# Kernel optimization log

Hardware: AMD Instinct MI355X
Metric: run time of the kernel (lower is better)

The kernel has to match this reference:

```python
import jax, jax.numpy as jnp
from jax import lax
import numpy as np


def _conv(x, w, b, stride=1, pad=1):
    # x: [B,C,H,W], w: [O,I,kh,kw]
    y = lax.conv_general_dilated(x, w, (stride, stride), [(pad, pad), (pad, pad)],
                                 dimension_numbers=('NCHW', 'OIHW', 'NCHW'))
    return y + b[None, :, None, None]


def _bn(x, g, b, eps=1e-5):
    # torch BatchNorm2d in training mode: per-channel batch stats, biased variance
    m = jnp.mean(x, axis=(0, 2, 3), keepdims=True)
    v = jnp.var(x, axis=(0, 2, 3), keepdims=True)
    return (x - m) * lax.rsqrt(v + eps) * g[None, :, None, None] + b[None, :, None, None]


def _res_stack(h, w1, b1, w2, b2):
    # one ResidualStack: layers of ReLU->conv3x3->ReLU->conv1x1 with skip, final ReLU
    for i in range(w1.shape[0]):
        t = jnp.maximum(_conv(jnp.maximum(h, 0.0), w1[i], b1[i], 1, 1), 0.0)
        h = h + _conv(t, w2[i], b2[i], 1, 0)
    return jnp.maximum(h, 0.0)


def reference(x, enc_conv0_w, enc_conv0_b, enc_bn0_g, enc_bn0_b, enc_conv1_w, enc_conv1_b,
              enc_bn1_g, enc_bn1_b, enc_conv2_w, enc_conv2_b, enc_res_w1, enc_res_b1,
              enc_res_w2, enc_res_b2, enc_conv3_w, enc_conv3_b, codebook,
              dec_conv0_w, dec_conv0_b, dec_res_w1, dec_res_b1, dec_res_w2, dec_res_b2,
              dec_conv1_w, dec_conv1_b, dec_deconv_w, dec_deconv_b):
    # ---- encoder ----
    h = jnp.maximum(_bn(_conv(x, enc_conv0_w, enc_conv0_b, 2, 1), enc_bn0_g, enc_bn0_b), 0.0)
    h = jnp.maximum(_bn(_conv(h, enc_conv1_w, enc_conv1_b, 1, 1), enc_bn1_g, enc_bn1_b), 0.0)
    h = _conv(h, enc_conv2_w, enc_conv2_b, 1, 1)
    for s in range(enc_res_w1.shape[0]):
        h = _res_stack(h, enc_res_w1[s], enc_res_b1[s], enc_res_w2[s], enc_res_b2[s])
    z = _conv(h, enc_conv3_w, enc_conv3_b, 1, 1)  # [B,D,H,W]
    # ---- vector quantizer ----
    Bz, D, H, W = z.shape
    zf = z.transpose(0, 2, 3, 1).reshape(-1, D)  # [N,D]
    d = (jnp.sum(zf * zf, axis=1, keepdims=True)
         - 2.0 * (zf @ codebook.T)
         + jnp.sum(codebook * codebook, axis=1))  # [N,K]
    idx = jnp.argmin(d, axis=1)
    q = codebook[idx]  # direct gather == one-hot @ codebook
    e_loss = jnp.mean((lax.stop_gradient(q) - zf) ** 2)
    q_loss = jnp.mean((q - lax.stop_gradient(zf)) ** 2)
    vq_loss = q_loss + 0.25 * e_loss
    qst = zf + lax.stop_gradient(q - zf)  # straight-through
    zq = qst.reshape(Bz, H, W, D).transpose(0, 3, 1, 2)
    # ---- decoder ----
    h = _conv(zq, dec_conv0_w, dec_conv0_b, 1, 1)
    for s in range(dec_res_w1.shape[0]):
        h = _res_stack(h, dec_res_w1[s], dec_res_b1[s], dec_res_w2[s], dec_res_b2[s])
    h = jnp.maximum(_conv(h, dec_conv1_w, dec_conv1_b, 1, 1), 0.0)
    # ConvTranspose2d(k=4,s=2,p=1): flip kernel, swap I/O, lhs_dilation=2, pad=k-1-p=2
    wt = jnp.transpose(jnp.flip(dec_deconv_w, (2, 3)), (1, 0, 2, 3))
    xr = lax.conv_general_dilated(h, wt, (1, 1), [(2, 2), (2, 2)], lhs_dilation=(2, 2),
                                  dimension_numbers=('NCHW', 'OIHW', 'NCHW'))
    xr = xr + dec_deconv_b[None, :, None, None]
    recon = jnp.mean((xr - x) ** 2)
    total = recon + vq_loss
    return xr, total, recon


def setup_inputs() -> dict:
    key = jax.random.key(0)
    ks = iter(jax.random.split(key, 64))

    def W(shape):
        fan_in = float(np.prod(shape[-3:]))
        return jax.random.normal(next(ks), shape, jnp.float32) / float(np.sqrt(fan_in))

    def Bv(shape):
        return 0.01 * jax.random.normal(next(ks), shape, jnp.float32)

    inp = {}
    inp['x'] = jax.random.normal(next(ks), (8, 3, 128, 128), jnp.float32)
    inp['enc_conv0_w'] = W((256, 3, 4, 4)); inp['enc_conv0_b'] = Bv((256,))
    inp['enc_bn0_g'] = 1.0 + 0.1 * jax.random.normal(next(ks), (256,), jnp.float32)
    inp['enc_bn0_b'] = Bv((256,))
    inp['enc_conv1_w'] = W((512, 256, 3, 3)); inp['enc_conv1_b'] = Bv((512,))
    inp['enc_bn1_g'] = 1.0 + 0.1 * jax.random.normal(next(ks), (512,), jnp.float32)
    inp['enc_bn1_b'] = Bv((512,))
    inp['enc_conv2_w'] = W((512, 512, 3, 3)); inp['enc_conv2_b'] = Bv((512,))
    inp['enc_res_w1'] = W((4, 4, 128, 512, 3, 3)); inp['enc_res_b1'] = Bv((4, 4, 128))
    inp['enc_res_w2'] = W((4, 4, 512, 128, 1, 1)); inp['enc_res_b2'] = Bv((4, 4, 512))
    inp['enc_conv3_w'] = W((256, 512, 3, 3)); inp['enc_conv3_b'] = Bv((256,))
    inp['codebook'] = jax.random.uniform(next(ks), (1024, 256), jnp.float32, -1.0 / 1024, 1.0 / 1024)
    inp['dec_conv0_w'] = W((512, 256, 3, 3)); inp['dec_conv0_b'] = Bv((512,))
    inp['dec_res_w1'] = W((4, 4, 128, 512, 3, 3)); inp['dec_res_b1'] = Bv((4, 4, 128))
    inp['dec_res_w2'] = W((4, 4, 512, 128, 1, 1)); inp['dec_res_b2'] = Bv((4, 4, 512))
    inp['dec_conv1_w'] = W((256, 512, 3, 3)); inp['dec_conv1_b'] = Bv((256,))
    inp['dec_deconv_w'] = W((256, 3, 4, 4)); inp['dec_deconv_b'] = Bv((3,))
    return inp
```

## Files before the change

kernel.cpp:

```cpp
#include <hip/hip_runtime.h>
#include <cstddef>

#define F_OUT_RELU   2
#define F_IN_BNORM   32
#define F_STATS      64

typedef __attribute__((ext_vector_type(8))) short short8;
typedef __attribute__((ext_vector_type(4))) short short4v;
typedef __attribute__((ext_vector_type(4))) float floatx4;

__device__ inline float bf2f(short h) {
  union { unsigned int u; float f; } v;
  v.u = ((unsigned int)(unsigned short)h) << 16;
  return v.f;
}
__device__ inline short f2bf(float f) {
  union { float f; unsigned int u; } v; v.f = f;
  unsigned int r = v.u + 0x7fffu + ((v.u >> 16) & 1u);
  return (short)(r >> 16);
}

__global__ void k_init(float* p) {
  for (int i = threadIdx.x; i < 1664; i += 256) p[i] = 0.f;
}

__global__ __launch_bounds__(256) void k_wswz(
    const float* __restrict__ w, short* __restrict__ wq,
    int Cin, int K2, int per_layer)
{
  int idx = blockIdx.x * 256 + threadIdx.x;
  if (idx >= per_layer) return;
  int layer = blockIdx.y;
  w  += (size_t)layer * per_layer;
  wq += (size_t)layer * per_layer;
  int nch = Cin >> 5;
  int j = idx & 7;
  int lane = (idx >> 3) & 63;
  int r = idx >> 9;
  int cich = r % nch; int r2 = r / nch;
  int kk = r2 % K2;   int co_grp = r2 / K2;
  int co = co_grp * 16 + (lane & 15);
  int ci = (cich << 5) + ((lane >> 4) << 3) + j;
  wq[idx] = f2bf(w[((size_t)co * Cin + ci) * K2 + kk]);
}

__global__ __launch_bounds__(256) void k_wswz0m(
    const float* __restrict__ w, short* __restrict__ wq)
{
  int idx = blockIdx.x * 256 + threadIdx.x;
  if (idx >= 16384) return;
  int co = idx >> 6, k = idx & 63;
  float val = (k < 48) ? w[co * 48 + k] : 0.f;
  int cich = k >> 5;
  int lane = (((k >> 3) & 3) << 4) | (co & 15);
  int j = k & 7;
  int cg = co >> 4;
  wq[((size_t)(cg * 2 + cich) * 64 + lane) * 8 + j] = f2bf(val);
}

__global__ __launch_bounds__(256) void k_im2col(
    const float* __restrict__ x, short* __restrict__ out)
{
  int idx = blockIdx.x * 256 + threadIdx.x;
  int k = idx & 63;
  int px = idx >> 6;
  int b = px >> 12;
  int rem = px & 4095;
  int y = rem >> 6, xc = rem & 63;
  int ci = k >> 4, t = k & 15;
  int ky = t >> 2, kx = t & 3;
  float v = 0.f;
  if (ci < 3) {
    int iy = 2 * y - 1 + ky, ix = 2 * xc - 1 + kx;
    if ((unsigned)iy < 128u && (unsigned)ix < 128u)
      v = x[((b * 3 + ci) * 128 + iy) * 128 + ix];
  }
  out[idx] = f2bf(v);
}

__global__ __launch_bounds__(256) void k_wswz_dd(
    const float* __restrict__ w, short* __restrict__ wdt)
{
  int idx = blockIdx.x * 256 + threadIdx.x;
  if (idx >= 12288) return;
  int ci = idx & 255, t = idx >> 8;
  int o = t % 3, kk = t / 3;
  wdt[idx] = f2bf(w[(ci * 3 + o) * 16 + kk]);
}

__global__ __launch_bounds__(256) void k_ccn(
    const float* __restrict__ cb, float* __restrict__ cc)
{
  int code = blockIdx.x * 256 + threadIdx.x;
  const float4* r = (const float4*)(cb + (size_t)code * 256);
  float s = 0.f;
  for (int i = 0; i < 64; ++i) {
    float4 v = r[i];
    s += v.x * v.x + v.y * v.y + v.z * v.z + v.w * v.w;
  }
  cc[code] = s;
}

__global__ __launch_bounds__(512) void k_bnfin(
    const float* __restrict__ sums, const float* __restrict__ g,
    const float* __restrict__ beta, float* __restrict__ ss, int C)
{
  int c = threadIdx.x;
  if (c >= C) return;
  float m = sums[c] * (1.f / 32768.f);
  float var = sums[C + c] * (1.f / 32768.f) - m * m;
  float sc = g[c] * rsqrtf(var + 1e-5f);
  ss[c] = sc;
  ss[C + c] = beta[c] - m * sc;
}

template <int K>
__global__ __launch_bounds__(256) void k_mconv(
    const short* __restrict__ in, short* __restrict__ out,
    const float* __restrict__ ss_in, float* __restrict__ sums_out,
    const short* __restrict__ wq, const float* __restrict__ bias,
    int Cin, int Cout, int flags)
{
  constexpr int K2 = K * K;
  constexpr int XS = 40;
  constexpr int NR = (K == 3) ? 4 : 1;
  constexpr int NX = (K == 3) ? 66 : 128;
  __shared__ __align__(16) short s_in[NR * NX * XS];
  __shared__ float ssl[1024];

  int tid = threadIdx.x;
  int lane = tid & 63;
  int wave = tid >> 6;
  int m = lane & 15, quad = lane >> 4;
  int wr = wave >> 1, wc = wave & 1;
  int y2 = blockIdx.y * 2, b = blockIdx.z;
  int coblk = blockIdx.x;
  int nch = Cin >> 5;

  if (flags & F_IN_BNORM) {
    for (int u = tid; u < 2 * Cin; u += 256) ssl[u] = ss_in[u];
  }

  floatx4 acc[4][4];
  #pragma unroll
  for (int f = 0; f < 4; ++f)
    #pragma unroll
    for (int p = 0; p < 4; ++p) acc[f][p] = (floatx4){0.f, 0.f, 0.f, 0.f};

  for (int cich = 0; cich < nch; ++cich) {
    __syncthreads();
    if (K == 3) {
      for (int u = tid; u < 4 * 66 * 4; u += 256) {
        int o = u & 3; int t2 = u >> 2;
        int xp = t2 % 66; int row = t2 / 66;
        int gy = y2 - 1 + row, gx = xp - 1;
        int ch = (cich << 5) + (o << 3);
        short8 v = {0, 0, 0, 0, 0, 0, 0, 0};
        if ((unsigned)gy < 64u && (unsigned)gx < 64u)
          v = *(const short8*)&in[((size_t)((b * 64 + gy) * 64 + gx)) * Cin + ch];
        if (flags & F_IN_BNORM) {
          #pragma unroll
          for (int i = 0; i < 8; ++i) {
            float f2 = bf2f(v[i]) * ssl[ch + i] + ssl[Cin + ch + i];
            v[i] = f2bf(f2 > 0.f ? f2 : 0.f);
          }
        }
        *(short8*)&s_in[(row * 66 + xp) * XS + (o << 3)] = v;
      }
    } else {
      for (int u = tid; u < 512; u += 256) {
        int o = u & 3; int xp = u >> 2;
        short8 v = *(const short8*)&in[((size_t)((b * 64 + y2) * 64 + xp)) * Cin + (cich << 5) + (o << 3)];
        *(short8*)&s_in[xp * XS + (o << 3)] = v;
      }
    }
    __syncthreads();

    #pragma unroll
    for (int kk = 0; kk < K2; ++kk) {
      int ky = (K == 3) ? (kk / 3) : 0;
      int kx = (K == 3) ? (kk - ky * 3) : 0;
      short8 af[4];
      #pragma unroll
      for (int f = 0; f < 4; ++f) {
        int cg = coblk * 8 + wc * 4 + f;
        af[f] = *(const short8*)&wq[(((size_t)(cg * K2 + kk) * nch + cich) * 64 + lane) * 8];
      }
      #pragma unroll
      for (int p = 0; p < 4; ++p) {
        short8 bv;
        if (K == 3)
          bv = *(const short8*)&s_in[((wr + ky) * 66 + p * 16 + m + kx) * XS + (quad << 3)];
        else
          bv = *(const short8*)&s_in[(wr * 64 + p * 16 + m) * XS + (quad << 3)];
        #pragma unroll
        for (int f = 0; f < 4; ++f)
          acc[f][p] = __builtin_amdgcn_mfma_f32_16x16x32_bf16(af[f], bv, acc[f][p], 0, 0, 0);
      }
    }
  }

  int pixrow = (b * 64 + y2 + wr) * 64;

  #pragma unroll
  for (int f = 0; f < 4; ++f) {
    int co4 = coblk * 128 + wc * 64 + f * 16 + quad * 4;
    floatx4 bv4 = *(const floatx4*)&bias[co4];
    float sv1[4] = {0.f, 0.f, 0.f, 0.f};
    float sv2[4] = {0.f, 0.f, 0.f, 0.f};
    #pragma unroll
    for (int p = 0; p < 4; ++p) {
      int x = p * 16 + m;
      size_t oidx = (size_t)(pixrow + x) * Cout + co4;
      float v[4];
      #pragma unroll
      for (int r = 0; r < 4; ++r) v[r] = acc[f][p][r] + bv4[r];
      if (flags & F_OUT_RELU) {
        #pragma unroll
        for (int r = 0; r < 4; ++r) v[r] = v[r] > 0.f ? v[r] : 0.f;
      }
      if (flags & F_STATS) {
        #pragma unroll
        for (int r = 0; r < 4; ++r) { sv1[r] += v[r]; sv2[r] += v[r] * v[r]; }
      }
      short4v sv;
      #pragma unroll
      for (int r = 0; r < 4; ++r) sv[r] = f2bf(v[r]);
      *(short4v*)&out[oidx] = sv;
    }
    if (flags & F_STATS) {
      #pragma unroll
      for (int r = 0; r < 4; ++r) {
        float a = sv1[r], a2 = sv2[r];
        #pragma unroll
        for (int off = 1; off <= 8; off <<= 1) {
          a += __shfl_xor(a, off);
          a2 += __shfl_xor(a2, off);
        }
        if (m == 0) {
          atomicAdd(&sums_out[co4 + r], a);
          atomicAdd(&sums_out[Cout + co4 + r], a2);
        }
      }
    }
  }
}

__global__ __launch_bounds__(512) void k_res(
    const short* __restrict__ hin, short* __restrict__ hout,
    const short* __restrict__ w1q, const float* __restrict__ b1,
    const short* __restrict__ w2q, const float* __restrict__ b2,
    int relu_out)
{
  constexpr int XS = 40;
  constexpr int TS = 136;
  __shared__ __align__(16) short s_in[4 * 66 * XS];
  __shared__ __align__(16) short t_tile[128 * TS];

  int tid = threadIdx.x;
  int lane = tid & 63;
  int wave = tid >> 6;
  int m = lane & 15, quad = lane >> 4;
  int wr = wave >> 2;
  int wq_ = wave & 3;
  int y2 = blockIdx.x * 2, b = blockIdx.y;

  floatx4 acc[2][4];
  #pragma unroll
  for (int f = 0; f < 2; ++f)
    #pragma unroll
    for (int p = 0; p < 4; ++p) acc[f][p] = (floatx4){0.f, 0.f, 0.f, 0.f};

  for (int cich = 0; cich < 16; ++cich) {
    __syncthreads();
    for (int u = tid; u < 4 * 66 * 4; u += 512) {
      int o = u & 3; int t2 = u >> 2;
      int xp = t2 % 66; int row = t2 / 66;
      int gy = y2 - 1 + row, gx = xp - 1;
      short8 v = {0, 0, 0, 0, 0, 0, 0, 0};
      if ((unsigned)gy < 64u && (unsigned)gx < 64u)
        v = *(const short8*)&hin[((size_t)((b * 64 + gy) * 64 + gx)) * 512 + (cich << 5) + (o << 3)];
      #pragma unroll
      for (int i = 0; i < 8; ++i) if (v[i] < 0) v[i] = 0;
      *(short8*)&s_in[(row * 66 + xp) * XS + (o << 3)] = v;
    }
    __syncthreads();

    #pragma unroll
    for (int kk = 0; kk < 9; ++kk) {
      int ky = kk / 3, kx = kk - ky * 3;
      short8 af[2];
      #pragma unroll
      for (int f = 0; f < 2; ++f) {
        int cg = wq_ * 2 + f;
        af[f] = *(const short8*)&w1q[(((size_t)(cg * 9 + kk) * 16 + cich) * 64 + lane) * 8];
      }
      #pragma unroll
      for (int p = 0; p < 4; ++p) {
        short8 bv = *(const short8*)&s_in[((wr + ky) * 66 + p * 16 + m + kx) * XS + (quad << 3)];
        #pragma unroll
        for (int f = 0; f < 2; ++f)
          acc[f][p] = __builtin_amdgcn_mfma_f32_16x16x32_bf16(af[f], bv, acc[f][p], 0, 0, 0);
      }
    }
  }

  __syncthreads();
  #pragma unroll
  for (int f = 0; f < 2; ++f) {
    int co4 = wq_ * 32 + f * 16 + quad * 4;
    floatx4 b4 = *(const floatx4*)&b1[co4];
    #pragma unroll
    for (int p = 0; p < 4; ++p) {
      int pxg = wr * 64 + p * 16 + m;
      short4v sv;
      #pragma unroll
      for (int r = 0; r < 4; ++r) {
        float v = acc[f][p][r] + b4[r];
        sv[r] = f2bf(v > 0.f ? v : 0.f);
      }
      *(short4v*)&t_tile[pxg * TS + co4] = sv;
    }
  }
  __syncthreads();

  floatx4 acc2[8][4];
  #pragma unroll
  for (int f = 0; f < 8; ++f)
    #pragma unroll
    for (int p = 0; p < 4; ++p) acc2[f][p] = (floatx4){0.f, 0.f, 0.f, 0.f};

  #pragma unroll
  for (int cich = 0; cich < 4; ++cich) {
    short8 bv2[4];
    #pragma unroll
    for (int p = 0; p < 4; ++p)
      bv2[p] = *(const short8*)&t_tile[(wr * 64 + p * 16 + m) * TS + (cich << 5) + (quad << 3)];
    #pragma unroll
    for (int f = 0; f < 8; ++f) {
      int cg2 = wq_ * 8 + f;
      short8 af2 = *(const short8*)&w2q[(((size_t)cg2 * 4 + cich) * 64 + lane) * 8];
      #pragma unroll
      for (int p = 0; p < 4; ++p)
        acc2[f][p] = __builtin_amdgcn_mfma_f32_16x16x32_bf16(af2, bv2[p], acc2[f][p], 0, 0, 0);
    }
  }

  int pixrow = (b * 64 + y2 + wr) * 64;
  #pragma unroll
  for (int f = 0; f < 8; ++f) {
    int co4 = wq_ * 128 + f * 16 + quad * 4;
    floatx4 b4 = *(const floatx4*)&b2[co4];
    #pragma unroll
    for (int p = 0; p < 4; ++p) {
      int x = p * 16 + m;
      size_t oidx = (size_t)(pixrow + x) * 512 + co4;
      short4v rr = *(const short4v*)&hin[oidx];
      short4v sv;
      #pragma unroll
      for (int r = 0; r < 4; ++r) {
        float v = acc2[f][p][r] + b4[r] + bf2f(rr[r]);
        if (relu_out) v = v > 0.f ? v : 0.f;
        sv[r] = f2bf(v);
      }
      *(short4v*)&hout[oidx] = sv;
    }
  }
}

__global__ __launch_bounds__(128) void k_vqm(
    const short* __restrict__ z, const short* __restrict__ cbq,
    const float* __restrict__ cb, const float* __restrict__ cc,
    short* __restrict__ zq, float* __restrict__ vq_sum)
{
  __shared__ __align__(16) short zl[64 * 264];
  __shared__ float ccl[1024];
  __shared__ int widx[64];
  __shared__ float red[128];

  int tid = threadIdx.x;
  int lane = tid & 63, wave = tid >> 6;
  int m = lane & 15, quad = lane >> 4;
  size_t px0 = (size_t)blockIdx.x * 64;

  for (int u = tid; u < 64 * 32; u += 128) {
    int px = u >> 5, o = u & 31;
    *(short8*)&zl[px * 264 + o * 8] = *(const short8*)&z[(px0 + px) * 256 + o * 8];
  }
  for (int u = tid; u < 1024; u += 128) ccl[u] = cc[u];
  __syncthreads();

  short8 bf[2][8];
  #pragma unroll
  for (int f = 0; f < 2; ++f) {
    int px = wave * 32 + f * 16 + m;
    #pragma unroll
    for (int kc = 0; kc < 8; ++kc)
      bf[f][kc] = *(const short8*)&zl[px * 264 + kc * 32 + quad * 8];
  }

  float best[2] = {3.4e38f, 3.4e38f};
  int bid[2] = {0, 0};

  for (int cg = 0; cg < 64; ++cg) {
    floatx4 acc0 = (floatx4){0.f, 0.f, 0.f, 0.f};
    floatx4 acc1 = (floatx4){0.f, 0.f, 0.f, 0.f};
    #pragma unroll
    for (int kc = 0; kc < 8; ++kc) {
      short8 af = *(const short8*)&cbq[((size_t)(cg * 8 + kc) * 64 + lane) * 8];
      acc0 = __builtin_amdgcn_mfma_f32_16x16x32_bf16(af, bf[0][kc], acc0, 0, 0, 0);
      acc1 = __builtin_amdgcn_mfma_f32_16x16x32_bf16(af, bf[1][kc], acc1, 0, 0, 0);
    }
    floatx4 c4 = *(const floatx4*)&ccl[cg * 16 + quad * 4];
    #pragma unroll
    for (int r = 0; r < 4; ++r) {
      int code = cg * 16 + quad * 4 + r;
      float s0 = c4[r] - 2.f * acc0[r];
      float s1 = c4[r] - 2.f * acc1[r];
      if (s0 < best[0]) { best[0] = s0; bid[0] = code; }
      if (s1 < best[1]) { best[1] = s1; bid[1] = code; }
    }
  }

  #pragma unroll
  for (int f = 0; f < 2; ++f) {
    float s = best[f]; int i = bid[f];
    #pragma unroll
    for (int off = 16; off <= 32; off <<= 1) {
      float s2 = __shfl_xor(s, off);
      int i2 = __shfl_xor(i, off);
      if (s2 < s || (s2 == s && i2 < i)) { s = s2; i = i2; }
    }
    if (quad == 0) widx[wave * 32 + f * 16 + m] = i;
  }
  __syncthreads();

  float local = 0.f;
  for (int px = 0; px < 64; ++px) {
    int code = widx[px];
    #pragma unroll
    for (int k = 0; k < 2; ++k) {
      int d = tid + k * 128;
      float q = cb[(size_t)code * 256 + d];
      float zv = bf2f(zl[px * 264 + d]);
      float df = q - zv;
      local += df * df;
      zq[(px0 + px) * 256 + d] = f2bf(q);
    }
  }
  red[tid] = local;
  __syncthreads();
  for (int off = 64; off > 0; off >>= 1) {
    if (tid < off) red[tid] += red[tid + off];
    __syncthreads();
  }
  if (tid == 0) atomicAdd(vq_sum, red[0]);
}

__global__ __launch_bounds__(256) void k_deconv(
    const short* __restrict__ h, const short* __restrict__ wdt,
    const float* __restrict__ bias, const float* __restrict__ x,
    float* __restrict__ xr, float* __restrict__ recon_sum)
{
  __shared__ float red[256];
  int idx = blockIdx.x * 256 + threadIdx.x;
  int xc = idx & 127;
  int yc = (idx >> 7) & 127;
  int b = idx >> 14;

  int vy[2], vky[2], nvy = 0;
  int ky0 = (yc + 1) & 1;
  #pragma unroll
  for (int t = 0; t < 2; ++t) {
    int ky = ky0 + 2 * t;
    int iy = (yc + 1 - ky) >> 1;
    if (iy >= 0 && iy < 64) { vky[nvy] = ky; vy[nvy] = iy; ++nvy; }
  }
  int vx[2], vkx[2], nvx = 0;
  int kx0 = (xc + 1) & 1;
  #pragma unroll
  for (int t = 0; t < 2; ++t) {
    int kx = kx0 + 2 * t;
    int ix = (xc + 1 - kx) >> 1;
    if (ix >= 0 && ix < 64) { vkx[nvx] = kx; vx[nvx] = ix; ++nvx; }
  }

  float acc[3] = {bias[0], bias[1], bias[2]};
  for (int ty = 0; ty < nvy; ++ty)
    for (int tx = 0; tx < nvx; ++tx) {
      int kk = vky[ty] * 4 + vkx[tx];
      const short* hp = h + ((size_t)((b * 64 + vy[ty]) * 64 + vx[tx])) * 256;
      const short* wp = wdt + kk * 768;
      for (int c = 0; c < 256; c += 8) {
        short8 hv = *(const short8*)&hp[c];
        short8 w0 = *(const short8*)&wp[c];
        short8 w1 = *(const short8*)&wp[256 + c];
        short8 w2 = *(const short8*)&wp[512 + c];
        #pragma unroll
        for (int i = 0; i < 8; ++i) {
          float hf = bf2f(hv[i]);
          acc[0] += hf * bf2f(w0[i]);
          acc[1] += hf * bf2f(w1[i]);
          acc[2] += hf * bf2f(w2[i]);
        }
      }
    }

  float local = 0.f;
  #pragma unroll
  for (int o = 0; o < 3; ++o) {
    size_t oi = ((size_t)(b * 3 + o) * 128 + yc) * 128 + xc;
    xr[oi] = acc[o];
    float df = acc[o] - x[oi];
    local += df * df;
  }
  red[threadIdx.x] = local;
  __syncthreads();
  for (int off = 128; off > 0; off >>= 1) {
    if (threadIdx.x < off) red[threadIdx.x] += red[threadIdx.x + off];
    __syncthreads();
  }
  if (threadIdx.x == 0) atomicAdd(recon_sum, red[0]);
}

__global__ void k_finalize(const float* __restrict__ a, float* __restrict__ out)
{
  float e = a[0] * (1.f / (32768.f * 256.f));
  float recon = a[1] * (1.f / 393216.f);
  out[393216] = recon + 1.25f * e;
  out[393217] = recon;
}

extern "C" void kernel_launch(void* const* d_in, const int* in_sizes, int n_in,
                              void* d_out, int out_size, void* d_ws, size_t ws_size,
                              hipStream_t stream)
{
  const float* x    = (const float*)d_in[0];
  const float* ec0w = (const float*)d_in[1];
  const float* ec0b = (const float*)d_in[2];
  const float* bn0g = (const float*)d_in[3];
  const float* bn0b = (const float*)d_in[4];
  const float* ec1w = (const float*)d_in[5];
  const float* ec1b = (const float*)d_in[6];
  const float* bn1g = (const float*)d_in[7];
  const float* bn1b = (const float*)d_in[8];
  const float* ec2w = (const float*)d_in[9];
  const float* ec2b = (const float*)d_in[10];
  const float* erw1 = (const float*)d_in[11];
  const float* erb1 = (const float*)d_in[12];
  const float* erw2 = (const float*)d_in[13];
  const float* erb2 = (const float*)d_in[14];
  const float* ec3w = (const float*)d_in[15];
  const float* ec3b = (const float*)d_in[16];
  const float* cb   = (const float*)d_in[17];
  const float* dc0w = (const float*)d_in[18];
  const float* dc0b = (const float*)d_in[19];
  const float* drw1 = (const float*)d_in[20];
  const float* drb1 = (const float*)d_in[21];
  const float* drw2 = (const float*)d_in[22];
  const float* drb2 = (const float*)d_in[23];
  const float* dc1w = (const float*)d_in[24];
  const float* dc1b = (const float*)d_in[25];
  const float* ddw  = (const float*)d_in[26];
  const float* ddb  = (const float*)d_in[27];

  short* wsu = (short*)d_ws;
  short* wq_ec1 = wsu;
  short* wq_ec2 = wsu + 1179648;
  short* wq_ec3 = wsu + 3538944;
  short* wq_dc0 = wsu + 4718592;
  short* wq_dc1 = wsu + 5898240;
  short* wq_er1 = wsu + 7077888;
  short* wq_er2 = wsu + 16515072;
  short* wq_dr1 = wsu + 17563648;
  short* wq_dr2 = wsu + 27000832;
  short* wq_dd  = wsu + 28049408;
  short* cbq    = wsu + 28061696;
  short* wq0    = wsu + 28323840;
  short* im2c   = wsu + 28340224;
  short* bufA   = wsu + 30437376;
  short* bufB   = wsu + 47214592;
  short* bufZ   = wsu + 63991808;
  float* stats  = (float*)(wsu + 80769024);
  float* bn0_sums = stats;
  float* bn1_sums = stats + 512;
  float* accums   = stats + 1536;
  float* bn0_ss   = stats + 1664;
  float* bn1_ss   = stats + 2176;
  float* ccn      = stats + 3200;

  k_init<<<1, 256, 0, stream>>>(stats);

  k_wswz0m<<<64, 256, 0, stream>>>(ec0w, wq0);
  k_wswz_dd<<<48, 256, 0, stream>>>(ddw, wq_dd);
  k_ccn<<<4, 256, 0, stream>>>(cb, ccn);
  k_wswz<<<1024, 256, 0, stream>>>(cb, cbq, 256, 1, 262144);
  k_wswz<<<4608, 256, 0, stream>>>(ec1w, wq_ec1, 256, 9, 1179648);
  k_wswz<<<9216, 256, 0, stream>>>(ec2w, wq_ec2, 512, 9, 2359296);
  k_wswz<<<4608, 256, 0, stream>>>(ec3w, wq_ec3, 512, 9, 1179648);
  k_wswz<<<4608, 256, 0, stream>>>(dc0w, wq_dc0, 256, 9, 1179648);
  k_wswz<<<4608, 256, 0, stream>>>(dc1w, wq_dc1, 512, 9, 1179648);
  k_wswz<<<dim3(2304, 16), 256, 0, stream>>>(erw1, wq_er1, 512, 9, 589824);
  k_wswz<<<dim3(256, 16), 256, 0, stream>>>(erw2, wq_er2, 128, 1, 65536);
  k_wswz<<<dim3(2304, 16), 256, 0, stream>>>(drw1, wq_dr1, 512, 9, 589824);
  k_wswz<<<dim3(256, 16), 256, 0, stream>>>(drw2, wq_dr2, 128, 1, 65536);

  k_im2col<<<8192, 256, 0, stream>>>(x, im2c);
  k_mconv<1><<<dim3(2, 32, 8), 256, 0, stream>>>(im2c, bufA, nullptr, bn0_sums,
                                                 wq0, ec0b, 64, 256, F_STATS);
  k_bnfin<<<1, 512, 0, stream>>>(bn0_sums, bn0g, bn0b, bn0_ss, 256);
  k_mconv<3><<<dim3(4, 32, 8), 256, 0, stream>>>(bufA, bufB, bn0_ss, bn1_sums,
                                                 wq_ec1, ec1b, 256, 512,
                                                 F_IN_BNORM | F_STATS);
  k_bnfin<<<1, 512, 0, stream>>>(bn1_sums, bn1g, bn1b, bn1_ss, 512);
  k_mconv<3><<<dim3(4, 32, 8), 256, 0, stream>>>(bufB, bufA, bn1_ss, nullptr,
                                                 wq_ec2, ec2b, 512, 512, F_IN_BNORM);

  {
    short* cur = bufA; short* alt = bufB;
    for (int l = 0; l < 16; ++l) {
      k_res<<<dim3(32, 8), 512, 0, stream>>>(cur, alt,
                                             wq_er1 + (size_t)l * 589824, erb1 + l * 128,
                                             wq_er2 + (size_t)l * 65536, erb2 + l * 512,
                                             ((l & 3) == 3) ? 1 : 0);
      short* tmp = cur; cur = alt; alt = tmp;
    }
  }
  k_mconv<3><<<dim3(2, 32, 8), 256, 0, stream>>>(bufA, bufZ, nullptr, nullptr,
                                                 wq_ec3, ec3b, 512, 256, 0);

  k_vqm<<<512, 128, 0, stream>>>(bufZ, cbq, cb, ccn, bufB, accums + 0);

  k_mconv<3><<<dim3(4, 32, 8), 256, 0, stream>>>(bufB, bufA, nullptr, nullptr,
                                                 wq_dc0, dc0b, 256, 512, 0);
  {
    short* cur = bufA; short* alt = bufB;
    for (int l = 0; l < 16; ++l) {
      k_res<<<dim3(32, 8), 512, 0, stream>>>(cur, alt,
                                             wq_dr1 + (size_t)l * 589824, drb1 + l * 128,
                                             wq_dr2 + (size_t)l * 65536, drb2 + l * 512,
                                             ((l & 3) == 3) ? 1 : 0);
      short* tmp = cur; cur = alt; alt = tmp;
    }
  }
  k_mconv<3><<<dim3(2, 32, 8), 256, 0, stream>>>(bufA, bufB, nullptr, nullptr,
                                                 wq_dc1, dc1b, 512, 256, F_OUT_RELU);

  k_deconv<<<512, 256, 0, stream>>>(bufB, wq_dd, ddb, x, (float*)d_out, accums + 1);
  k_finalize<<<1, 1, 0, stream>>>(accums, (float*)d_out);
}
```

Baseline: 3.990 ms.

## Double conv tile rows and input-channel chunk in mconv and res kernels

k_mconv now runs 512 threads and covers four output rows per block instead of two, so each staged 3x3 halo tile is shared by more output rows and less redundant halo data is loaded. Both k_mconv and k_res stage 64 input channels per shared-memory load instead of 32, halving the number of barrier-separated load phases. The cost is larger shared-memory tiles (padded row stride 72), which may lower occupancy, and weight fragments are still read from global memory on every step.

```diff
diff --git a/kernel.cpp b/kernel.cpp
--- a/kernel.cpp
+++ b/kernel.cpp
@@ -115,17 +115,17 @@
 }
 
 template <int K>
-__global__ __launch_bounds__(256) void k_mconv(
+__global__ __launch_bounds__(512) void k_mconv(
     const short* __restrict__ in, short* __restrict__ out,
     const float* __restrict__ ss_in, float* __restrict__ sums_out,
     const short* __restrict__ wq, const float* __restrict__ bias,
     int Cin, int Cout, int flags)
 {
   constexpr int K2 = K * K;
-  constexpr int XS = 40;
-  constexpr int NR = (K == 3) ? 4 : 1;
-  constexpr int NX = (K == 3) ? 66 : 128;
-  __shared__ __align__(16) short s_in[NR * NX * XS];
+  constexpr int XS = 72;
+  constexpr int NROW = (K == 3) ? 6 : 4;
+  constexpr int NX = (K == 3) ? 66 : 64;
+  __shared__ __align__(16) short s_in[NROW * NX * XS];
   __shared__ float ssl[1024];
 
   int tid = threadIdx.x;
@@ -133,12 +133,13 @@
   int wave = tid >> 6;
   int m = lane & 15, quad = lane >> 4;
   int wr = wave >> 1, wc = wave & 1;
-  int y2 = blockIdx.y * 2, b = blockIdx.z;
+  int y4 = blockIdx.y * 4, b = blockIdx.z;
   int coblk = blockIdx.x;
   int nch = Cin >> 5;
+  int nch2 = Cin >> 6;
 
   if (flags & F_IN_BNORM) {
-    for (int u = tid; u < 2 * Cin; u += 256) ssl[u] = ss_in[u];
+    for (int u = tid; u < 2 * Cin; u += 512) ssl[u] = ss_in[u];
   }
 
   floatx4 acc[4][4];
@@ -147,14 +148,14 @@
     #pragma unroll
     for (int p = 0; p < 4; ++p) acc[f][p] = (floatx4){0.f, 0.f, 0.f, 0.f};
 
-  for (int cich = 0; cich < nch; ++cich) {
+  for (int cich2 = 0; cich2 < nch2; ++cich2) {
     __syncthreads();
     if (K == 3) {
-      for (int u = tid; u < 4 * 66 * 4; u += 256) {
-        int o = u & 3; int t2 = u >> 2;
+      for (int u = tid; u < 6 * 66 * 8; u += 512) {
+        int o = u & 7; int t2 = u >> 3;
         int xp = t2 % 66; int row = t2 / 66;
-        int gy = y2 - 1 + row, gx = xp - 1;
-        int ch = (cich << 5) + (o << 3);
+        int gy = y4 - 1 + row, gx = xp - 1;
+        int ch = (cich2 << 6) + (o << 3);
         short8 v = {0, 0, 0, 0, 0, 0, 0, 0};
         if ((unsigned)gy < 64u && (unsigned)gx < 64u)
           v = *(const short8*)&in[((size_t)((b * 64 + gy) * 64 + gx)) * Cin + ch];
@@ -168,10 +169,12 @@
         *(short8*)&s_in[(row * 66 + xp) * XS + (o << 3)] = v;
       }
     } else {
-      for (int u = tid; u < 512; u += 256) {
-        int o = u & 3; int xp = u >> 2;
-        short8 v = *(const short8*)&in[((size_t)((b * 64 + y2) * 64 + xp)) * Cin + (cich << 5) + (o << 3)];
-        *(short8*)&s_in[xp * XS + (o << 3)] = v;
+      for (int u = tid; u < 4 * 64 * 8; u += 512) {
+        int o = u & 7; int t2 = u >> 3;
+        int xp = t2 & 63; int row = t2 >> 6;
+        int ch = (cich2 << 6) + (o << 3);
+        short8 v = *(const short8*)&in[((size_t)((b * 64 + y4 + row) * 64 + xp)) * Cin + ch];
+        *(short8*)&s_in[(row * 64 + xp) * XS + (o << 3)] = v;
       }
     }
     __syncthreads();
@@ -180,27 +183,31 @@
     for (int kk = 0; kk < K2; ++kk) {
       int ky = (K == 3) ? (kk / 3) : 0;
       int kx = (K == 3) ? (kk - ky * 3) : 0;
-      short8 af[4];
-      #pragma unroll
-      for (int f = 0; f < 4; ++f) {
-        int cg = coblk * 8 + wc * 4 + f;
-        af[f] = *(const short8*)&wq[(((size_t)(cg * K2 + kk) * nch + cich) * 64 + lane) * 8];
-      }
-      #pragma unroll
-      for (int p = 0; p < 4; ++p) {
-        short8 bv;
-        if (K == 3)
-          bv = *(const short8*)&s_in[((wr + ky) * 66 + p * 16 + m + kx) * XS + (quad << 3)];
-        else
-          bv = *(const short8*)&s_in[(wr * 64 + p * 16 + m) * XS + (quad << 3)];
-        #pragma unroll
-        for (int f = 0; f < 4; ++f)
-          acc[f][p] = __builtin_amdgcn_mfma_f32_16x16x32_bf16(af[f], bv, acc[f][p], 0, 0, 0);
-      }
-    }
-  }
-
-  int pixrow = (b * 64 + y2 + wr) * 64;
+      #pragma unroll
+      for (int s = 0; s < 2; ++s) {
+        int cich = cich2 * 2 + s;
+        short8 af[4];
+        #pragma unroll
+        for (int f = 0; f < 4; ++f) {
+          int cg = coblk * 8 + wc * 4 + f;
+          af[f] = *(const short8*)&wq[(((size_t)(cg * K2 + kk) * nch + cich) * 64 + lane) * 8];
+        }
+        #pragma unroll
+        for (int p = 0; p < 4; ++p) {
+          short8 bv;
+          if (K == 3)
+            bv = *(const short8*)&s_in[((wr + ky) * 66 + p * 16 + m + kx) * XS + s * 32 + (quad << 3)];
+          else
+            bv = *(const short8*)&s_in[(wr * 64 + p * 16 + m) * XS + s * 32 + (quad << 3)];
+          #pragma unroll
+          for (int f = 0; f < 4; ++f)
+            acc[f][p] = __builtin_amdgcn_mfma_f32_16x16x32_bf16(af[f], bv, acc[f][p], 0, 0, 0);
+        }
+      }
+    }
+  }
+
+  int pixrow = (b * 64 + y4 + wr) * 64;
 
   #pragma unroll
   for (int f = 0; f < 4; ++f) {
@@ -252,7 +259,7 @@
     const short* __restrict__ w2q, const float* __restrict__ b2,
     int relu_out)
 {
-  constexpr int XS = 40;
+  constexpr int XS = 72;
   constexpr int TS = 136;
   __shared__ __align__(16) short s_in[4 * 66 * XS];
   __shared__ __align__(16) short t_tile[128 * TS];
@@ -271,15 +278,16 @@
     #pragma unroll
     for (int p = 0; p < 4; ++p) acc[f][p] = (floatx4){0.f, 0.f, 0.f, 0.f};
 
-  for (int cich = 0; cich < 16; ++cich) {
+  for (int cich2 = 0; cich2 < 8; ++cich2) {
     __syncthreads();
-    for (int u = tid; u < 4 * 66 * 4; u += 512) {
-      int o = u & 3; int t2 = u >> 2;
+    for (int u = tid; u < 4 * 66 * 8; u += 512) {
+      int o = u & 7; int t2 = u >> 3;
       int xp = t2 % 66; int row = t2 / 66;
       int gy = y2 - 1 + row, gx = xp - 1;
+      int ch = (cich2 << 6) + (o << 3);
       short8 v = {0, 0, 0, 0, 0, 0, 0, 0};
       if ((unsigned)gy < 64u && (unsigned)gx < 64u)
-        v = *(const short8*)&hin[((size_t)((b * 64 + gy) * 64 + gx)) * 512 + (cich << 5) + (o << 3)];
+        v = *(const short8*)&hin[((size_t)((b * 64 + gy) * 64 + gx)) * 512 + ch];
       #pragma unroll
       for (int i = 0; i < 8; ++i) if (v[i] < 0) v[i] = 0;
       *(short8*)&s_in[(row * 66 + xp) * XS + (o << 3)] = v;
@@ -289,18 +297,22 @@
     #pragma unroll
     for (int kk = 0; kk < 9; ++kk) {
       int ky = kk / 3, kx = kk - ky * 3;
-      short8 af[2];
-      #pragma unroll
-      for (int f = 0; f < 2; ++f) {
-        int cg = wq_ * 2 + f;
-        af[f] = *(const short8*)&w1q[(((size_t)(cg * 9 + kk) * 16 + cich) * 64 + lane) * 8];
-      }
-      #pragma unroll
-      for (int p = 0; p < 4; ++p) {
-        short8 bv = *(const short8*)&s_in[((wr + ky) * 66 + p * 16 + m + kx) * XS + (quad << 3)];
-        #pragma unroll
-        for (int f = 0; f < 2; ++f)
-          acc[f][p] = __builtin_amdgcn_mfma_f32_16x16x32_bf16(af[f], bv, acc[f][p], 0, 0, 0);
+      #pragma unroll
+      for (int s = 0; s < 2; ++s) {
+        int cich = cich2 * 2 + s;
+        short8 af[2];
+        #pragma unroll
+        for (int f = 0; f < 2; ++f) {
+          int cg = wq_ * 2 + f;
+          af[f] = *(const short8*)&w1q[(((size_t)(cg * 9 + kk) * 16 + cich) * 64 + lane) * 8];
+        }
+        #pragma unroll
+        for (int p = 0; p < 4; ++p) {
+          short8 bv = *(const short8*)&s_in[((wr + ky) * 66 + p * 16 + m + kx) * XS + s * 32 + (quad << 3)];
+          #pragma unroll
+          for (int f = 0; f < 2; ++f)
+            acc[f][p] = __builtin_amdgcn_mfma_f32_16x16x32_bf16(af[f], bv, acc[f][p], 0, 0, 0);
+        }
       }
     }
   }
@@ -606,14 +618,14 @@
   k_wswz<<<dim3(256, 16), 256, 0, stream>>>(drw2, wq_dr2, 128, 1, 65536);
 
   k_im2col<<<8192, 256, 0, stream>>>(x, im2c);
-  k_mconv<1><<<dim3(2, 32, 8), 256, 0, stream>>>(im2c, bufA, nullptr, bn0_sums,
+  k_mconv<1><<<dim3(2, 16, 8), 512, 0, stream>>>(im2c, bufA, nullptr, bn0_sums,
                                                  wq0, ec0b, 64, 256, F_STATS);
   k_bnfin<<<1, 512, 0, stream>>>(bn0_sums, bn0g, bn0b, bn0_ss, 256);
-  k_mconv<3><<<dim3(4, 32, 8), 256, 0, stream>>>(bufA, bufB, bn0_ss, bn1_sums,
+  k_mconv<3><<<dim3(4, 16, 8), 512, 0, stream>>>(bufA, bufB, bn0_ss, bn1_sums,
                                                  wq_ec1, ec1b, 256, 512,
                                                  F_IN_BNORM | F_STATS);
   k_bnfin<<<1, 512, 0, stream>>>(bn1_sums, bn1g, bn1b, bn1_ss, 512);
-  k_mconv<3><<<dim3(4, 32, 8), 256, 0, stream>>>(bufB, bufA, bn1_ss, nullptr,
+  k_mconv<3><<<dim3(4, 16, 8), 512, 0, stream>>>(bufB, bufA, bn1_ss, nullptr,
                                                  wq_ec2, ec2b, 512, 512, F_IN_BNORM);
 
   {
@@ -626,12 +638,12 @@
       short* tmp = cur; cur = alt; alt = tmp;
     }
   }
-  k_mconv<3><<<dim3(2, 32, 8), 256, 0, stream>>>(bufA, bufZ, nullptr, nullptr,
+  k_mconv<3><<<dim3(2, 16, 8), 512, 0, stream>>>(bufA, bufZ, nullptr, nullptr,
                                                  wq_ec3, ec3b, 512, 256, 0);
 
   k_vqm<<<512, 128, 0, stream>>>(bufZ, cbq, cb, ccn, bufB, accums + 0);
 
-  k_mconv<3><<<dim3(4, 32, 8), 256, 0, stream>>>(bufB, bufA, nullptr, nullptr,
+  k_mconv<3><<<dim3(4, 16, 8), 512, 0, stream>>>(bufB, bufA, nullptr, nullptr,
                                                  wq_dc0, dc0b, 256, 512, 0);
   {
     short* cur = bufA; short* alt = bufB;
@@ -643,7 +655,7 @@
       short* tmp = cur; cur = alt; alt = tmp;
     }
   }
-  k_mconv<3><<<dim3(2, 32, 8), 256, 0, stream>>>(bufA, bufB, nullptr, nullptr,
+  k_mconv<3><<<dim3(2, 16, 8), 512, 0, stream>>>(bufA, bufB, nullptr, nullptr,
                                                  wq_dc1, dc1b, 512, 256, F_OUT_RELU);
 
   k_deconv<<<512, 256, 0, stream>>>(bufB, wq_dd, ddb, x, (float*)d_out, accums + 1);
```

After: 3.992 ms. Within noise of the previous version (+0.0%).
